# Kernel optimization log

Hardware: AMD Instinct MI355X
Metric: run time of the kernel (lower is better)

The kernel has to match this reference:

```python
import jax, jax.numpy as jnp
import numpy as np

DEPTH = 12  # perfect binary tree: 2**DEPTH - 1 internal nodes, 2**DEPTH leaf children


def setup_inputs() -> dict:
    key = jax.random.key(0)
    k0, k1, k2, k3, k4 = jax.random.split(key, 5)
    H = 1024   # hidden_size
    I = 1024   # input_size
    N = 2 ** DEPTH - 1  # internal nodes, heap order (root = 0)
    scale = 0.02  # keep gates out of saturation
    emb = jax.random.normal(k0, (N, I), jnp.float32)
    W_ih = jax.random.normal(k1, (8 * H, I), jnp.float32) * scale
    W_hh = jax.random.normal(k2, (8 * H, 2 * H), jnp.float32) * scale
    b_ih = jax.random.normal(k3, (8 * H,), jnp.float32) * scale
    b_hh = jax.random.normal(k4, (8 * H,), jnp.float32) * scale
    return {"emb": emb, "W_ih": W_ih, "W_hh": W_hh, "b_ih": b_ih, "b_hh": b_hh}


def reference(emb, W_ih, W_hh, b_ih, b_hh):
    # Batched-by-level Tree-LSTM over a perfect binary tree in heap order.
    # nn.LSTM hidden size is 2H; node state passed upward is the first H dims.
    H2 = W_hh.shape[1]          # 2 * hidden_size
    H = H2 // 2
    b = b_ih + b_hh
    # Leaves: hidden = cell = zeros((1, H)) per the module's base case.
    h = jnp.zeros((2 ** DEPTH, H), emb.dtype)
    c = jnp.zeros((2 ** DEPTH, H), emb.dtype)
    for k in range(DEPTH - 1, -1, -1):  # bottom-up over levels
        n = 2 ** k
        # cat((a.hidden, b.hidden), dim=1): children of node j are 2j, 2j+1
        h_cat = h.reshape(n, H2)
        c_cat = c.reshape(n, H2)
        x = emb[n - 1: 2 * n - 1]  # level-k embeddings (heap indices n-1 .. 2n-2)
        gates = x @ W_ih.T + h_cat @ W_hh.T + b  # (n, 8H)
        i_, f_, g_, o_ = jnp.split(gates, 4, axis=1)  # PyTorch gate order i,f,g,o
        c_new = jax.nn.sigmoid(f_) * c_cat + jax.nn.sigmoid(i_) * jnp.tanh(g_)
        h_new = jax.nn.sigmoid(o_) * jnp.tanh(c_new)
        h = h_new[:, :H]  # slice back to hidden_size, as the module does
        c = c_new[:, :H]
    # root hidden and cell, each (1, H)
    return jnp.concatenate([h, c], axis=1)
```

## Files before the change

### kernel.cpp

```cpp
#include <hip/hip_runtime.h>
#include <hip/hip_bf16.h>
#include <math.h>


#define TREE_DEPTH 12

typedef unsigned short u16;
typedef unsigned int u32;
typedef __attribute__((ext_vector_type(8))) short bf16x8;
typedef __attribute__((ext_vector_type(4))) float f32x4;
typedef __attribute__((ext_vector_type(8))) unsigned short u16x8;
typedef __attribute__((ext_vector_type(2))) unsigned int u32x2;

__device__ __forceinline__ void gload16(const void* g, void* l) {
    __builtin_amdgcn_global_load_lds(
        (const __attribute__((address_space(1))) u32*)g,
        (__attribute__((address_space(3))) u32*)l, 16, 0, 0);
}

__device__ __forceinline__ u16 f2bf(float f) {
    __hip_bfloat16 h = __float2bfloat16(f);
    return *reinterpret_cast<u16*>(&h);
}
__device__ __forceinline__ u16 f2h(float f) {
    _Float16 h = (_Float16)f;
    return *reinterpret_cast<u16*>(&h);
}
__device__ __forceinline__ float h2f(u16 u) {
    _Float16 h;
    *reinterpret_cast<u16*>(&h) = u;
    return (float)h;
}
__device__ __forceinline__ float fsig(float x) {
    return 1.0f / (1.0f + __expf(-x));
}
__device__ __forceinline__ float ftanh(float x) {
    return 1.0f - 2.0f / (1.0f + __expf(2.0f * x));
}

__global__ void prep(const float* __restrict__ Wih,
                     const float* __restrict__ Whh,
                     const float* __restrict__ emb,
                     const float* __restrict__ b_ih,
                     const float* __restrict__ b_hh,
                     u16* __restrict__ Wih_p, u16* __restrict__ Whh_p,
                     u16* __restrict__ xb, float* __restrict__ bge) {
    const int bid = blockIdx.x;
    if (bid < 12288) {
        const int b = bid & 4095;
        const int seg = bid >> 12;
        const int x = b & 7, t = b >> 3;
        const int e = ((t & 3) * 8 + x) * 128 + (t >> 2);
        const int g = (e >> 4) & 3;
        const int j = (e >> 6) * 16 + (e & 15);
        const int wr = g * 2048 + j;
        const int col = threadIdx.x * 4;
        f32x4 v;
        u16* dst;
        if (seg == 0) {
            v = __builtin_nontemporal_load(
                (const f32x4*)(Wih + (size_t)wr * 1024 + col));
            dst = Wih_p + (size_t)e * 1024 + col;
        } else {
            v = __builtin_nontemporal_load(
                (const f32x4*)(Whh + (size_t)wr * 2048 + (seg - 1) * 1024 + col));
            dst = Whh_p + (size_t)e * 2048 + (seg - 1) * 1024 + col;
        }
        u32x2 p;
        p[0] = (u32)f2bf(v[0]) | ((u32)f2bf(v[1]) << 16);
        p[1] = (u32)f2bf(v[2]) | ((u32)f2bf(v[3]) << 16);
        *reinterpret_cast<u32x2*>(dst) = p;
    } else if (bid < 16383) {
        size_t idx = ((size_t)(bid - 12288) * 256 + threadIdx.x) * 4;
        f32x4 v = __builtin_nontemporal_load((const f32x4*)(emb + idx));
        u32x2 p;
        p[0] = (u32)f2bf(v[0]) | ((u32)f2bf(v[1]) << 16);
        p[1] = (u32)f2bf(v[2]) | ((u32)f2bf(v[3]) << 16);
        *reinterpret_cast<u32x2*>(xb + idx) = p;
    } else {
        int e = (bid - 16383) * 256 + threadIdx.x;
        int g = (e >> 4) & 3;
        int j = (e >> 6) * 16 + (e & 15);
        int r = g * 2048 + j;
        bge[e] = b_ih[r] + b_hh[r];
    }
}

__global__ __launch_bounds__(256) void gemm_gx(
    const u16* __restrict__ xb, const u16* __restrict__ Wp,
    const float* __restrict__ bge, u16* __restrict__ GX,
    u16* __restrict__ hdst, float* __restrict__ cdst)
{
    __shared__ u16 smem[128 * 140];

    const int gx_ = gridDim.x;
    int b = blockIdx.x + gx_ * blockIdx.y;
    const int x = b & 7, t = b >> 3;
    const int ct = (t & 3) * 8 + x;
    const int mt = t >> 2;
    const int m0 = mt * 128, c0 = ct * 128;

    const int tid = threadIdx.x, lane = tid & 63, w = tid >> 6;
    const int wr = (w >> 1) * 64, wc = (w & 1) * 64;

    f32x4 acc[4][4];
    #pragma unroll
    for (int i = 0; i < 4; ++i)
        #pragma unroll
        for (int j = 0; j < 4; ++j)
            acc[i][j] = f32x4{0.f, 0.f, 0.f, 0.f};

    const u16* gp[8];
    u16* dl[8];
    #pragma unroll
    for (int i = 0; i < 8; ++i) {
        const int s = tid + i * 256;
        const int r = s >> 3;
        const int o = (s & 7) * 16;
        const int ke = (o ^ ((r & 7) << 4)) >> 1;
        gp[i] = (r < 128) ? xb + (size_t)(m0 + r) * 1024 + ke
                          : Wp + (size_t)(c0 + r - 128) * 1024 + ke;
        dl[i] = smem + s * 8;
    }

    const int fl = lane & 15;
    const int kunit = (lane >> 4) * 16;

    for (int k0 = 0; k0 < 1024; k0 += 64) {
        #pragma unroll
        for (int i = 0; i < 8; ++i) { gload16(gp[i], dl[i]); gp[i] += 64; }
        __syncthreads();
        #pragma unroll
        for (int ks = 0; ks < 2; ++ks) {
            bf16x8 a_[4], b_[4];
            #pragma unroll
            for (int i = 0; i < 4; ++i) {
                const int ar = wr + i * 16 + fl;
                const int byo = (ks * 64 + kunit) ^ ((ar & 7) << 4);
                a_[i] = *reinterpret_cast<const bf16x8*>(
                    reinterpret_cast<const char*>(smem + ar * 64) + byo);
            }
            #pragma unroll
            for (int j = 0; j < 4; ++j) {
                const int br = 128 + wc + j * 16 + fl;
                const int byo = (ks * 64 + kunit) ^ ((br & 7) << 4);
                b_[j] = *reinterpret_cast<const bf16x8*>(
                    reinterpret_cast<const char*>(smem + br * 64) + byo);
            }
            #pragma unroll
            for (int i = 0; i < 4; ++i)
                #pragma unroll
                for (int j = 0; j < 4; ++j)
                    acc[i][j] = __builtin_amdgcn_mfma_f32_16x16x32_bf16(
                        a_[i], b_[j], acc[i][j], 0, 0, 0);
        }
        __syncthreads();
    }

    const int rg = (lane >> 4) * 4;
    if (m0 < 2047) {
        #pragma unroll
        for (int i = 0; i < 4; ++i)
            #pragma unroll
            for (int j = 0; j < 4; ++j) {
                const float bv = bge[c0 + wc + j * 16 + fl];
                #pragma unroll
                for (int r = 0; r < 4; ++r)
                    smem[(wr + i * 16 + rg + r) * 140 + (wc + j * 16 + fl)] =
                        f2h(acc[i][j][r] + bv);
            }
        __syncthreads();
        const int row_ = tid >> 4, chunk = tid & 15;
        #pragma unroll
        for (int it = 0; it < 8; ++it) {
            const int row = it * 16 + row_;
            if (m0 + row < 2047) {
                u16x8 v = *reinterpret_cast<const u16x8*>(
                    &smem[row * 140 + chunk * 8]);
                __builtin_nontemporal_store(
                    v, (u16x8*)(GX + (size_t)(m0 + row) * 4096 + c0 + chunk * 8));
            }
        }
    }
    if (m0 + 127 >= 2047) {
        const int jj = ((c0 + wc) >> 6) * 16 + fl;
        const float bi  = bge[c0 + wc + fl];
        const float bgg = bge[c0 + wc + 32 + fl];
        const float bo  = bge[c0 + wc + 48 + fl];
        #pragma unroll
        for (int i = 0; i < 4; ++i) {
            #pragma unroll
            for (int r = 0; r < 4; ++r) {
                const int m = m0 + wr + i * 16 + rg + r;
                if (m < 2047 || m >= 4095) continue;
                const int mm = m - 2047;
                const float cn = fsig(acc[i][0][r] + bi) * ftanh(acc[i][2][r] + bgg);
                const float hn = fsig(acc[i][3][r] + bo) * ftanh(cn);
                hdst[(size_t)(mm >> 1) * 2048 + (mm & 1) * 1024 + jj] = f2bf(hn);
                if (!(mm & 1))
                    cdst[(size_t)(mm >> 1) * 1024 + jj] = cn;
            }
        }
    }
}

template <int MI, int MW, int NW, int KG>
__global__ __launch_bounds__(MW* NW* KG * 64) void fused_level(
    const u16* __restrict__ A, const u16* __restrict__ Wp,
    const u16* __restrict__ GXl, const float* __restrict__ cprev,
    u16* __restrict__ hnext, float* __restrict__ cnext,
    float* __restrict__ outp, int n)
{
    constexpr int BM = MI * 16 * MW;
    constexpr int BN = NW * 64;
    constexpr int S = MW * NW;
    constexpr int NFR = MI * 4;
    constexpr int RC = NFR > 8 ? 8 : NFR;
    constexpr int NP = NFR / RC;
    constexpr int ROWS = BM + BN;
    constexpr int SLOTS = ROWS * 8;
    constexpr int GT = S * 64;
    constexpr int NL = SLOTS / GT;
    static_assert(SLOTS % GT == 0, "slot mapping must be exact");
    constexpr int STG = KG * ROWS * 128;
    constexpr int REDB = (KG > 1) ? (KG - 1) * S * RC * 64 * 16 : 0;
    constexpr int SMEM = STG > REDB ? STG : REDB;
    __shared__ __align__(16) char smem[SMEM];

    const int gx_ = gridDim.x;
    int b = blockIdx.x + gx_ * blockIdx.y;
    const int x = b & 7;
    int t = b >> 3;
    int ct, mt;
    if constexpr (NW == 2) {
        ct = (t & 3) * 8 + x; mt = t >> 2;
    } else {
        const int lo = t & 1; t >>= 1;
        ct = ((t & 3) * 8 + x) * 2 + lo; mt = t >> 2;
    }
    const int m0 = mt * BM;
    const int c0 = ct * BN;

    const int tid = threadIdx.x;
    const int lane = tid & 63;
    const int w = tid >> 6;
    const int kg = w / S;
    const int slot = w % S;
    const int wm = slot / NW;
    const int wn = slot % NW;

    const int Kc = 2048 / KG;
    const int kbeg = kg * Kc;

    u16* buf = (u16*)smem + (size_t)kg * ROWS * 64;

    const int gtid = slot * 64 + lane;
    const u16* gp[NL];
    u16* dl[NL];
    #pragma unroll
    for (int i = 0; i < NL; ++i) {
        const int s = gtid + i * GT;
        const int r = s >> 3;
        const int o = (s & 7) * 16;
        const int ke = (o ^ ((r & 7) << 4)) >> 1;
        if (r < BM) {
            int ar = m0 + r;
            if (ar >= n) ar = n - 1;
            gp[i] = A + (size_t)ar * 2048 + kbeg + ke;
        } else {
            gp[i] = Wp + (size_t)(c0 + r - BM) * 2048 + kbeg + ke;
        }
        dl[i] = buf + s * 8;
    }

    f32x4 acc[MI][4];
    #pragma unroll
    for (int mi = 0; mi < MI; ++mi)
        #pragma unroll
        for (int f = 0; f < 4; ++f)
            acc[mi][f] = f32x4{0.f, 0.f, 0.f, 0.f};

    const int fl = lane & 15;
    const int kunit = (lane >> 4) * 16;
    const int ar0 = wm * MI * 16;
    const int bc0 = BM;

    for (int k0 = 0; k0 < Kc; k0 += 64) {
        #pragma unroll
        for (int i = 0; i < NL; ++i) { gload16(gp[i], dl[i]); gp[i] += 64; }
        __syncthreads();
        #pragma unroll
        for (int ks = 0; ks < 2; ++ks) {
            bf16x8 a_[MI], b_[4];
            #pragma unroll
            for (int mi = 0; mi < MI; ++mi) {
                const int ar = ar0 + mi * 16 + fl;
                const int byo = (ks * 64 + kunit) ^ ((ar & 7) << 4);
                a_[mi] = *reinterpret_cast<const bf16x8*>(
                    reinterpret_cast<const char*>(buf + ar * 64) + byo);
            }
            #pragma unroll
            for (int f = 0; f < 4; ++f) {
                const int br = bc0 + wn * 64 + f * 16 + fl;
                const int byo = (ks * 64 + kunit) ^ ((br & 7) << 4);
                b_[f] = *reinterpret_cast<const bf16x8*>(
                    reinterpret_cast<const char*>(buf + br * 64) + byo);
            }
            #pragma unroll
            for (int mi = 0; mi < MI; ++mi)
                #pragma unroll
                for (int f = 0; f < 4; ++f)
                    acc[mi][f] = __builtin_amdgcn_mfma_f32_16x16x32_bf16(
                        a_[mi], b_[f], acc[mi][f], 0, 0, 0);
        }
        __syncthreads();
    }

    if constexpr (KG > 1) {
        f32x4* red = reinterpret_cast<f32x4*>(smem);
        #pragma unroll
        for (int pass = 0; pass < NP; ++pass) {
            if (kg > 0) {
                #pragma unroll
                for (int f = 0; f < RC; ++f) {
                    const int fr = pass * RC + f;
                    red[(((kg - 1) * S + slot) * RC + f) * 64 + lane] =
                        acc[fr >> 2][fr & 3];
                }
            }
            __syncthreads();
            if (kg == 0) {
                #pragma unroll
                for (int q = 1; q < KG; ++q)
                    #pragma unroll
                    for (int f = 0; f < RC; ++f) {
                        const int fr = pass * RC + f;
                        f32x4 v = red[(((q - 1) * S + slot) * RC + f) * 64 + lane];
                        acc[fr >> 2][fr & 3][0] += v[0];
                        acc[fr >> 2][fr & 3][1] += v[1];
                        acc[fr >> 2][fr & 3][2] += v[2];
                        acc[fr >> 2][fr & 3][3] += v[3];
                    }
            }
            __syncthreads();
        }
    }

    if (kg != 0) return;
    const int j = ((c0 + wn * 64) >> 6) * 16 + fl;
    #pragma unroll
    for (int mi = 0; mi < MI; ++mi) {
        #pragma unroll
        for (int r = 0; r < 4; ++r) {
            const int m = m0 + wm * MI * 16 + mi * 16 + (lane >> 4) * 4 + r;
            if (m >= n) continue;
            const u16* gx = GXl + (size_t)m * 4096 + c0 + wn * 64 + fl;
            const float i_ = acc[mi][0][r] + h2f(__builtin_nontemporal_load(gx));
            const float f_ = acc[mi][1][r] + h2f(__builtin_nontemporal_load(gx + 16));
            const float g_ = acc[mi][2][r] + h2f(__builtin_nontemporal_load(gx + 32));
            const float o_ = acc[mi][3][r] + h2f(__builtin_nontemporal_load(gx + 48));
            const float cc = __builtin_nontemporal_load(cprev + (size_t)m * 1024 + j);
            const float cn = fsig(f_) * cc + fsig(i_) * ftanh(g_);
            const float hn = fsig(o_) * ftanh(cn);
            if (hnext)
                hnext[(size_t)(m >> 1) * 2048 + (m & 1) * 1024 + j] = f2bf(hn);
            if (!(m & 1))
                __builtin_nontemporal_store(cn, cnext + (size_t)(m >> 1) * 1024 + j);
            if (outp) { outp[j] = hn; outp[1024 + j] = cn; }
        }
    }
}

extern "C" void kernel_launch(void* const* d_in, const int* in_sizes, int n_in,
                              void* d_out, int out_size, void* d_ws, size_t ws_size,
                              hipStream_t stream) {
    const float* emb  = (const float*)d_in[0];
    const float* W_ih = (const float*)d_in[1];
    const float* W_hh = (const float*)d_in[2];
    const float* b_ih = (const float*)d_in[3];
    const float* b_hh = (const float*)d_in[4];
    float* out = (float*)d_out;

    char* p = (char*)d_ws;
    float* bge  = (float*)p;  p += 16384;
    u16* Wih_p  = (u16*)p;    p += (size_t)4096 * 1024 * 2;
    u16* Whh_p  = (u16*)p;    p += (size_t)4096 * 2048 * 2;
    u16* xb     = (u16*)p;    p += (size_t)4096 * 1024 * 2;
    u16* GX     = (u16*)p;    p += (size_t)4096 * 4096 * 2;
    u16* Hcat   = (u16*)p;    p += (size_t)4096 * 2048 * 2;
    float* cbA  = (float*)p;  p += (size_t)1024 * 1024 * 4;
    float* cbB  = (float*)p;  p += (size_t)1024 * 1024 * 4;

    prep<<<16399, 256, 0, stream>>>(W_ih, W_hh, emb, b_ih, b_hh,
                                    Wih_p, Whh_p, xb, bge);

    #define OFF(k) (4096 - (2 << (k)))

    gemm_gx<<<dim3(32, 32), 256, 0, stream>>>(
        xb, Wih_p, bge, GX, Hcat + (size_t)OFF(10) * 2048, cbA);

    const float* cprev = cbA;
    float* cbufs[2] = {cbB, cbA};
    int t = 0;
    for (int k = TREE_DEPTH - 2; k >= 0; --k) {
        const int n = 1 << k;
        const u16* A = Hcat + (size_t)OFF(k) * 2048;
        const u16* GXl = GX + (size_t)(n - 1) * 4096;
        u16* hnext = (k > 0) ? (Hcat + (size_t)OFF(k - 1) * 2048) : nullptr;
        float* cnext = cbufs[t];
        float* outp = (k == 0) ? out : nullptr;

        if (k == 10) {
            fused_level<4, 1, 2, 2><<<dim3(16, 32), 256, 0, stream>>>(
                A, Whh_p, GXl, cprev, hnext, cnext, outp, n);
        } else if (k == 9) {
            fused_level<2, 1, 2, 2><<<dim3(16, 32), 256, 0, stream>>>(
                A, Whh_p, GXl, cprev, hnext, cnext, outp, n);
        } else if (k == 8) {
            fused_level<1, 1, 1, 4><<<dim3(16, 64), 256, 0, stream>>>(
                A, Whh_p, GXl, cprev, hnext, cnext, outp, n);
        } else {
            const int gx = (n >= 16) ? n / 16 : 1;
            fused_level<1, 1, 1, 8><<<dim3(gx, 64), 512, 0, stream>>>(
                A, Whh_p, GXl, cprev, hnext, cnext, outp, n);
        }
        cprev = cnext; t ^= 1;
    }
}
```

Baseline: 221.0 us.

## Double-buffer LDS tiles in gemm_gx to overlap global loads with MFMA

Splits shared memory into two 64 KB-sized halves and prefetches the next K-tile via global_load_lds into the alternate buffer while computing on the current one. Explicit vmcnt waits and raw s_barriers with scheduling fences replace __syncthreads so only the previous stage's loads are awaited. This targets load latency stalls in the input-projection GEMM but doubles LDS usage, which may reduce occupancy.

New measurement: 222.3 us. About the same (+0.6%).

```diff
diff --git a/kernel.cpp b/kernel.cpp
--- a/kernel.cpp
+++ b/kernel.cpp
@@ -16,6 +16,16 @@
     __builtin_amdgcn_global_load_lds(
         (const __attribute__((address_space(1))) u32*)g,
         (__attribute__((address_space(3))) u32*)l, 16, 0, 0);
+}
+
+template <int N>
+__device__ __forceinline__ void vmwait() {
+    asm volatile("s_waitcnt vmcnt(%0)" :: "n"(N) : "memory");
+}
+__device__ __forceinline__ void rbar() {
+    __builtin_amdgcn_sched_barrier(0);
+    __builtin_amdgcn_s_barrier();
+    __builtin_amdgcn_sched_barrier(0);
 }
 
 __device__ __forceinline__ u16 f2bf(float f) {
@@ -91,7 +101,7 @@
     const float* __restrict__ bge, u16* __restrict__ GX,
     u16* __restrict__ hdst, float* __restrict__ cdst)
 {
-    __shared__ u16 smem[128 * 140];
+    __shared__ u16 smem[32768];
 
     const int gx_ = gridDim.x;
     int b = blockIdx.x + gx_ * blockIdx.y;
@@ -110,8 +120,10 @@
         for (int j = 0; j < 4; ++j)
             acc[i][j] = f32x4{0.f, 0.f, 0.f, 0.f};
 
+    u16* bufs[2] = {smem, smem + 16384};
     const u16* gp[8];
-    u16* dl[8];
+    u16* dl0[8];
+    u16* dl1[8];
     #pragma unroll
     for (int i = 0; i < 8; ++i) {
         const int s = tid + i * 256;
@@ -120,42 +132,61 @@
         const int ke = (o ^ ((r & 7) << 4)) >> 1;
         gp[i] = (r < 128) ? xb + (size_t)(m0 + r) * 1024 + ke
                           : Wp + (size_t)(c0 + r - 128) * 1024 + ke;
-        dl[i] = smem + s * 8;
+        dl0[i] = bufs[0] + s * 8;
+        dl1[i] = bufs[1] + s * 8;
     }
 
     const int fl = lane & 15;
     const int kunit = (lane >> 4) * 16;
 
-    for (int k0 = 0; k0 < 1024; k0 += 64) {
-        #pragma unroll
-        for (int i = 0; i < 8; ++i) { gload16(gp[i], dl[i]); gp[i] += 64; }
-        __syncthreads();
-        #pragma unroll
-        for (int ks = 0; ks < 2; ++ks) {
-            bf16x8 a_[4], b_[4];
-            #pragma unroll
-            for (int i = 0; i < 4; ++i) {
-                const int ar = wr + i * 16 + fl;
-                const int byo = (ks * 64 + kunit) ^ ((ar & 7) << 4);
-                a_[i] = *reinterpret_cast<const bf16x8*>(
-                    reinterpret_cast<const char*>(smem + ar * 64) + byo);
-            }
-            #pragma unroll
-            for (int j = 0; j < 4; ++j) {
-                const int br = 128 + wc + j * 16 + fl;
-                const int byo = (ks * 64 + kunit) ^ ((br & 7) << 4);
-                b_[j] = *reinterpret_cast<const bf16x8*>(
-                    reinterpret_cast<const char*>(smem + br * 64) + byo);
-            }
-            #pragma unroll
-            for (int i = 0; i < 4; ++i)
-                #pragma unroll
-                for (int j = 0; j < 4; ++j)
-                    acc[i][j] = __builtin_amdgcn_mfma_f32_16x16x32_bf16(
-                        a_[i], b_[j], acc[i][j], 0, 0, 0);
-        }
-        __syncthreads();
-    }
+    #define STAGE0() { _Pragma("unroll") \
+        for (int i = 0; i < 8; ++i) { gload16(gp[i], dl0[i]); gp[i] += 64; } }
+    #define STAGE1() { _Pragma("unroll") \
+        for (int i = 0; i < 8; ++i) { gload16(gp[i], dl1[i]); gp[i] += 64; } }
+
+    #define COMPUTE(B) {                                                     \
+        _Pragma("unroll")                                                    \
+        for (int ks = 0; ks < 2; ++ks) {                                     \
+            bf16x8 a_[4], b_[4];                                             \
+            _Pragma("unroll")                                                \
+            for (int i = 0; i < 4; ++i) {                                    \
+                const int ar = wr + i * 16 + fl;                             \
+                const int byo = (ks * 64 + kunit) ^ ((ar & 7) << 4);         \
+                a_[i] = *reinterpret_cast<const bf16x8*>(                    \
+                    reinterpret_cast<const char*>((B) + ar * 64) + byo);     \
+            }                                                                \
+            _Pragma("unroll")                                                \
+            for (int j = 0; j < 4; ++j) {                                    \
+                const int br = 128 + wc + j * 16 + fl;                       \
+                const int byo = (ks * 64 + kunit) ^ ((br & 7) << 4);         \
+                b_[j] = *reinterpret_cast<const bf16x8*>(                    \
+                    reinterpret_cast<const char*>((B) + br * 64) + byo);     \
+            }                                                                \
+            _Pragma("unroll")                                                \
+            for (int i = 0; i < 4; ++i)                                      \
+                _Pragma("unroll")                                            \
+                for (int j = 0; j < 4; ++j)                                  \
+                    acc[i][j] = __builtin_amdgcn_mfma_f32_16x16x32_bf16(     \
+                        a_[i], b_[j], acc[i][j], 0, 0, 0);                   \
+        } }
+
+    STAGE0();
+    #pragma unroll 2
+    for (int it = 0; it < 16; ++it) {
+        const int cur = it & 1;
+        if (it < 15) {
+            if (cur == 0) STAGE1() else STAGE0();
+            vmwait<8>();
+        } else {
+            vmwait<0>();
+        }
+        rbar();
+        if (cur == 0) COMPUTE(bufs[0]) else COMPUTE(bufs[1]);
+        rbar();
+    }
+    #undef STAGE0
+    #undef STAGE1
+    #undef COMPUTE
 
     const int rg = (lane >> 4) * 4;
     if (m0 < 2047) {
```

## Split K across grid z for small tree levels with separate activation tail kernel

Applied to the files above, without the earlier changes.

For the small upper levels (k<=5), the recurrent GEMM's K dimension is split across blockIdx.z (2 or 4 slices). Each slice writes fp32 partial gate sums to a workspace buffer, and a new act_tail kernel then sums the partials, adds the input-projection gates and applies the LSTM activations. The goal is to put more workgroups on the GPU when only a few rows remain, at the cost of one extra launch per level plus the round-trip of partial sums through global memory.

Measured after the change: 221.5 us. About the same (+0.2%).

```diff
diff --git a/kernel.cpp b/kernel.cpp
--- a/kernel.cpp
+++ b/kernel.cpp
@@ -204,12 +204,12 @@
     }
 }
 
-template <int MI, int MW, int NW, int KG>
+template <int MI, int MW, int NW, int KG, int KSX>
 __global__ __launch_bounds__(MW* NW* KG * 64) void fused_level(
     const u16* __restrict__ A, const u16* __restrict__ Wp,
     const u16* __restrict__ GXl, const float* __restrict__ cprev,
     u16* __restrict__ hnext, float* __restrict__ cnext,
-    float* __restrict__ outp, int n)
+    float* __restrict__ outp, int n, float* __restrict__ pout)
 {
     constexpr int BM = MI * 16 * MW;
     constexpr int BN = NW * 64;
@@ -249,8 +249,8 @@
     const int wm = slot / NW;
     const int wn = slot % NW;
 
-    const int Kc = 2048 / KG;
-    const int kbeg = kg * Kc;
+    const int Kc = (2048 / KSX) / KG;
+    const int kbeg = (int)blockIdx.z * (2048 / KSX) + kg * Kc;
 
     u16* buf = (u16*)smem + (size_t)kg * ROWS * 64;
 
@@ -347,6 +347,23 @@
     }
 
     if (kg != 0) return;
+
+    if constexpr (KSX > 1) {
+        float* po = pout + (size_t)blockIdx.z * n * 4096;
+        #pragma unroll
+        for (int mi = 0; mi < MI; ++mi)
+            #pragma unroll
+            for (int f = 0; f < 4; ++f)
+                #pragma unroll
+                for (int r = 0; r < 4; ++r) {
+                    const int m = m0 + wm * MI * 16 + mi * 16 + (lane >> 4) * 4 + r;
+                    if (m < n)
+                        po[(size_t)m * 4096 + c0 + wn * 64 + f * 16 + fl] =
+                            acc[mi][f][r];
+                }
+        return;
+    }
+
     const int j = ((c0 + wn * 64) >> 6) * 16 + fl;
     #pragma unroll
     for (int mi = 0; mi < MI; ++mi) {
@@ -371,6 +388,50 @@
     }
 }
 
+__global__ void act_tail(const float* __restrict__ parts, int ksn, size_t stride,
+                         const u16* __restrict__ GXl,
+                         const float* __restrict__ cprev,
+                         u16* __restrict__ hnext, float* __restrict__ cnext,
+                         float* __restrict__ outp, int n)
+{
+    int idx = blockIdx.x * 256 + threadIdx.x;
+    if (idx >= n * 256) return;
+    const int m = idx >> 8;
+    const int j4 = (idx & 255) * 4;
+    const int eb = (j4 >> 4) * 64 + (j4 & 15);
+
+    const u16* gx = GXl + (size_t)m * 4096;
+    float iv[4], fv[4], gv[4], ov[4];
+    #pragma unroll
+    for (int t = 0; t < 4; ++t) {
+        iv[t] = h2f(gx[eb + t]);
+        fv[t] = h2f(gx[eb + 16 + t]);
+        gv[t] = h2f(gx[eb + 32 + t]);
+        ov[t] = h2f(gx[eb + 48 + t]);
+    }
+    for (int s = 0; s < ksn; ++s) {
+        const float* p = parts + (size_t)s * stride + (size_t)m * 4096;
+        #pragma unroll
+        for (int t = 0; t < 4; ++t) {
+            iv[t] += p[eb + t];
+            fv[t] += p[eb + 16 + t];
+            gv[t] += p[eb + 32 + t];
+            ov[t] += p[eb + 48 + t];
+        }
+    }
+    #pragma unroll
+    for (int t = 0; t < 4; ++t) {
+        const float cc = cprev[(size_t)m * 1024 + j4 + t];
+        const float cn = fsig(fv[t]) * cc + fsig(iv[t]) * ftanh(gv[t]);
+        const float hn = fsig(ov[t]) * ftanh(cn);
+        if (hnext)
+            hnext[(size_t)(m >> 1) * 2048 + (m & 1) * 1024 + j4 + t] = f2bf(hn);
+        if (!(m & 1))
+            cnext[(size_t)(m >> 1) * 1024 + j4 + t] = cn;
+        if (outp) { outp[j4 + t] = hn; outp[1024 + j4 + t] = cn; }
+    }
+}
+
 extern "C" void kernel_launch(void* const* d_in, const int* in_sizes, int n_in,
                               void* d_out, int out_size, void* d_ws, size_t ws_size,
                               hipStream_t stream) {
@@ -390,6 +451,7 @@
     u16* Hcat   = (u16*)p;    p += (size_t)4096 * 2048 * 2;
     float* cbA  = (float*)p;  p += (size_t)1024 * 1024 * 4;
     float* cbB  = (float*)p;  p += (size_t)1024 * 1024 * 4;
+    float* parts = (float*)p; p += (size_t)4 * 32 * 4096 * 4;
 
     prep<<<16399, 256, 0, stream>>>(W_ih, W_hh, emb, b_ih, b_hh,
                                     Wih_p, Whh_p, xb, bge);
@@ -411,18 +473,29 @@
         float* outp = (k == 0) ? out : nullptr;
 
         if (k == 10) {
-            fused_level<4, 1, 2, 2><<<dim3(16, 32), 256, 0, stream>>>(
-                A, Whh_p, GXl, cprev, hnext, cnext, outp, n);
+            fused_level<4, 1, 2, 2, 1><<<dim3(16, 32), 256, 0, stream>>>(
+                A, Whh_p, GXl, cprev, hnext, cnext, outp, n, nullptr);
         } else if (k == 9) {
-            fused_level<2, 1, 2, 2><<<dim3(16, 32), 256, 0, stream>>>(
-                A, Whh_p, GXl, cprev, hnext, cnext, outp, n);
+            fused_level<2, 1, 2, 2, 1><<<dim3(16, 32), 256, 0, stream>>>(
+                A, Whh_p, GXl, cprev, hnext, cnext, outp, n, nullptr);
         } else if (k == 8) {
-            fused_level<1, 1, 1, 4><<<dim3(16, 64), 256, 0, stream>>>(
-                A, Whh_p, GXl, cprev, hnext, cnext, outp, n);
+            fused_level<1, 1, 1, 4, 1><<<dim3(16, 64), 256, 0, stream>>>(
+                A, Whh_p, GXl, cprev, hnext, cnext, outp, n, nullptr);
+        } else if (k >= 6) {
+            const int gxd = n / 16;
+            fused_level<1, 1, 1, 8, 1><<<dim3(gxd, 64), 512, 0, stream>>>(
+                A, Whh_p, GXl, cprev, hnext, cnext, outp, n, nullptr);
+        } else if (k == 5) {
+            fused_level<1, 1, 1, 8, 2><<<dim3(2, 64, 2), 512, 0, stream>>>(
+                A, Whh_p, nullptr, nullptr, nullptr, nullptr, nullptr, n, parts);
+            act_tail<<<n, 256, 0, stream>>>(parts, 2, (size_t)n * 4096,
+                                            GXl, cprev, hnext, cnext, outp, n);
         } else {
-            const int gx = (n >= 16) ? n / 16 : 1;
-            fused_level<1, 1, 1, 8><<<dim3(gx, 64), 512, 0, stream>>>(
-                A, Whh_p, GXl, cprev, hnext, cnext, outp, n);
+            const int gxd = (n >= 16) ? n / 16 : 1;
+            fused_level<1, 1, 1, 8, 4><<<dim3(gxd, 64, 4), 512, 0, stream>>>(
+                A, Whh_p, nullptr, nullptr, nullptr, nullptr, nullptr, n, parts);
+            act_tail<<<n, 256, 0, stream>>>(parts, 4, (size_t)n * 4096,
+                                            GXl, cprev, hnext, cnext, outp, n);
         }
         cprev = cnext; t ^= 1;
     }
```

## Overlap W_hh bf16 packing with input-projection GEMM in one launch

Applied to the files above, without the earlier changes.

The conversion of W_hh from fp32 to packed bf16 moves out of the prep kernel and into extra blocks appended to the input-projection GEMM launch. The memory-bound packing can then run alongside the compute-bound GEMM instead of serially before it. The GEMM grid becomes 1-D, and the extra blocks return early after converting one row segment. Block scheduling order may leave the packing blocks running after the GEMM tail, and shared-memory allocation applies to them as well, which could limit occupancy.

Measured after the change: 223.7 us. No clear change (+1.2%).

```diff
diff --git a/kernel.cpp b/kernel.cpp
--- a/kernel.cpp
+++ b/kernel.cpp
@@ -38,47 +38,36 @@
     return 1.0f - 2.0f / (1.0f + __expf(2.0f * x));
 }
 
-__global__ void prep(const float* __restrict__ Wih,
-                     const float* __restrict__ Whh,
-                     const float* __restrict__ emb,
-                     const float* __restrict__ b_ih,
-                     const float* __restrict__ b_hh,
-                     u16* __restrict__ Wih_p, u16* __restrict__ Whh_p,
-                     u16* __restrict__ xb, float* __restrict__ bge) {
+__global__ void prep_a(const float* __restrict__ Wih,
+                       const float* __restrict__ emb,
+                       const float* __restrict__ b_ih,
+                       const float* __restrict__ b_hh,
+                       u16* __restrict__ Wih_p,
+                       u16* __restrict__ xb, float* __restrict__ bge) {
     const int bid = blockIdx.x;
-    if (bid < 12288) {
-        const int b = bid & 4095;
-        const int seg = bid >> 12;
+    if (bid < 4096) {
+        const int b = bid;
         const int x = b & 7, t = b >> 3;
         const int e = ((t & 3) * 8 + x) * 128 + (t >> 2);
         const int g = (e >> 4) & 3;
         const int j = (e >> 6) * 16 + (e & 15);
         const int wr = g * 2048 + j;
         const int col = threadIdx.x * 4;
-        f32x4 v;
-        u16* dst;
-        if (seg == 0) {
-            v = __builtin_nontemporal_load(
-                (const f32x4*)(Wih + (size_t)wr * 1024 + col));
-            dst = Wih_p + (size_t)e * 1024 + col;
-        } else {
-            v = __builtin_nontemporal_load(
-                (const f32x4*)(Whh + (size_t)wr * 2048 + (seg - 1) * 1024 + col));
-            dst = Whh_p + (size_t)e * 2048 + (seg - 1) * 1024 + col;
-        }
+        f32x4 v = __builtin_nontemporal_load(
+            (const f32x4*)(Wih + (size_t)wr * 1024 + col));
         u32x2 p;
         p[0] = (u32)f2bf(v[0]) | ((u32)f2bf(v[1]) << 16);
         p[1] = (u32)f2bf(v[2]) | ((u32)f2bf(v[3]) << 16);
-        *reinterpret_cast<u32x2*>(dst) = p;
-    } else if (bid < 16383) {
-        size_t idx = ((size_t)(bid - 12288) * 256 + threadIdx.x) * 4;
+        *reinterpret_cast<u32x2*>(Wih_p + (size_t)e * 1024 + col) = p;
+    } else if (bid < 8191) {
+        size_t idx = ((size_t)(bid - 4096) * 256 + threadIdx.x) * 4;
         f32x4 v = __builtin_nontemporal_load((const f32x4*)(emb + idx));
         u32x2 p;
         p[0] = (u32)f2bf(v[0]) | ((u32)f2bf(v[1]) << 16);
         p[1] = (u32)f2bf(v[2]) | ((u32)f2bf(v[3]) << 16);
         *reinterpret_cast<u32x2*>(xb + idx) = p;
     } else {
-        int e = (bid - 16383) * 256 + threadIdx.x;
+        int e = (bid - 8191) * 256 + threadIdx.x;
         int g = (e >> 4) & 3;
         int j = (e >> 6) * 16 + (e & 15);
         int r = g * 2048 + j;
@@ -86,16 +75,35 @@
     }
 }
 
-__global__ __launch_bounds__(256) void gemm_gx(
+__global__ __launch_bounds__(256) void gx_pack(
     const u16* __restrict__ xb, const u16* __restrict__ Wp,
     const float* __restrict__ bge, u16* __restrict__ GX,
-    u16* __restrict__ hdst, float* __restrict__ cdst)
+    u16* __restrict__ hdst, float* __restrict__ cdst,
+    const float* __restrict__ Whh_f, u16* __restrict__ Whh_p)
 {
     __shared__ u16 smem[128 * 140];
 
-    const int gx_ = gridDim.x;
-    int b = blockIdx.x + gx_ * blockIdx.y;
-    const int x = b & 7, t = b >> 3;
+    const int bid = blockIdx.x;
+    if (bid >= 1024) {
+        const int b2 = bid - 1024;
+        const int seg = b2 >> 12;
+        const int b = b2 & 4095;
+        const int x = b & 7, t = b >> 3;
+        const int e = ((t & 3) * 8 + x) * 128 + (t >> 2);
+        const int g = (e >> 4) & 3;
+        const int j = (e >> 6) * 16 + (e & 15);
+        const int wr = g * 2048 + j;
+        const int col = threadIdx.x * 4;
+        f32x4 v = __builtin_nontemporal_load(
+            (const f32x4*)(Whh_f + (size_t)wr * 2048 + seg * 1024 + col));
+        u32x2 p;
+        p[0] = (u32)f2bf(v[0]) | ((u32)f2bf(v[1]) << 16);
+        p[1] = (u32)f2bf(v[2]) | ((u32)f2bf(v[3]) << 16);
+        *reinterpret_cast<u32x2*>(Whh_p + (size_t)e * 2048 + seg * 1024 + col) = p;
+        return;
+    }
+
+    const int x = bid & 7, t = bid >> 3;
     const int ct = (t & 3) * 8 + x;
     const int mt = t >> 2;
     const int m0 = mt * 128, c0 = ct * 128;
@@ -391,13 +399,12 @@
     float* cbA  = (float*)p;  p += (size_t)1024 * 1024 * 4;
     float* cbB  = (float*)p;  p += (size_t)1024 * 1024 * 4;
 
-    prep<<<16399, 256, 0, stream>>>(W_ih, W_hh, emb, b_ih, b_hh,
-                                    Wih_p, Whh_p, xb, bge);
+    prep_a<<<8207, 256, 0, stream>>>(W_ih, emb, b_ih, b_hh, Wih_p, xb, bge);
 
     #define OFF(k) (4096 - (2 << (k)))
 
-    gemm_gx<<<dim3(32, 32), 256, 0, stream>>>(
-        xb, Wih_p, bge, GX, Hcat + (size_t)OFF(10) * 2048, cbA);
+    gx_pack<<<9216, 256, 0, stream>>>(
+        xb, Wih_p, bge, GX, Hcat + (size_t)OFF(10) * 2048, cbA, W_hh, Whh_p);
 
     const float* cprev = cbA;
     float* cbufs[2] = {cbB, cbA};
```
